# Kernel optimization log

Measured on AMD Instinct MI355X. Metric: run time of the kernel, lower is better.

Reference implementation:

```python
import jax, jax.numpy as jnp
import numpy as np

WIN = (7, 7)
NUM_HEADS = 12
LORA_SCALING = 16.0 / 16.0  # lora_alpha / lora_rank


def _relative_position_index(win):
    wh, ww = win
    coords = np.stack(np.meshgrid(np.arange(wh), np.arange(ww), indexing='ij'))  # (2, wh, ww)
    cf = coords.reshape(2, -1)
    rel = cf[:, :, None] - cf[:, None, :]  # (2, N, N)
    rel = rel.transpose(1, 2, 0)
    rel[:, :, 0] += wh - 1
    rel[:, :, 1] += ww - 1
    rel[:, :, 0] *= 2 * ww - 1
    return jnp.asarray(rel.sum(-1), dtype=jnp.int32)  # (N, N)


def setup_inputs() -> dict:
    key = jax.random.key(0)
    ks = jax.random.split(key, 12)
    B_, N, C, r = 2048, 49, 384, 16
    nW = 64
    s = 0.02
    return {
        'x': jax.random.normal(ks[0], (B_, N, C), jnp.float32),
        'mask': jnp.zeros((nW, N, N), jnp.float32),
        'qkv_w': jax.random.normal(ks[1], (C, 3 * C), jnp.float32) * s,
        'qkv_b': jax.random.normal(ks[2], (3 * C,), jnp.float32) * s,
        'qa_w': jax.random.normal(ks[3], (C, r), jnp.float32) * s,
        'qb_w': jax.random.normal(ks[4], (r, C), jnp.float32) * s,
        'va_w': jax.random.normal(ks[5], (C, r), jnp.float32) * s,
        'vb_w': jax.random.normal(ks[6], (r, C), jnp.float32) * s,
        'rpb_table': jax.random.normal(ks[7], ((2 * WIN[0] - 1) * (2 * WIN[1] - 1), NUM_HEADS), jnp.float32) * s,
        'proj_w': jax.random.normal(ks[8], (C, C), jnp.float32) * s,
        'proj_b': jax.random.normal(ks[9], (C,), jnp.float32) * s,
    }


def reference(x, mask, qkv_w, qkv_b, qa_w, qb_w, va_w, vb_w, rpb_table, proj_w, proj_b):
    B_, N, C = x.shape
    H = NUM_HEADS
    hd = C // H
    scale = hd ** -0.5

    qkv = (x @ qkv_w + qkv_b).reshape(B_, N, 3, H, hd)
    qkv = jnp.transpose(qkv, (2, 0, 3, 1, 4))  # (3, B_, H, N, hd)
    q, k, v = qkv[0], qkv[1], qkv[2]

    q_lora = LORA_SCALING * ((x @ qa_w) @ qb_w)  # (B_, N, C)
    q = q + jnp.transpose(q_lora.reshape(B_, N, H, hd), (0, 2, 1, 3))
    v_lora = LORA_SCALING * ((x @ va_w) @ vb_w)
    v = v + jnp.transpose(v_lora.reshape(B_, N, H, hd), (0, 2, 1, 3))

    attn = jnp.einsum('bhnd,bhmd->bhnm', q * scale, k)  # (B_, H, N, N)

    rel_idx = _relative_position_index(WIN)  # (N, N) static int
    rpb = rpb_table[rel_idx]  # (N, N, H)
    attn = attn + jnp.transpose(rpb, (2, 0, 1))[None]

    nW = mask.shape[0]
    attn = attn.reshape(B_ // nW, nW, H, N, N) + mask[None, :, None]
    attn = attn.reshape(B_, H, N, N)
    attn = jax.nn.softmax(attn, axis=-1)

    out = jnp.einsum('bhnm,bhmd->bhnd', attn, v)
    out = jnp.transpose(out, (0, 2, 1, 3)).reshape(B_, N, C)
    return out @ proj_w + proj_b
```

## Files before the change

kernel.cpp:

```cpp
#include <hip/hip_runtime.h>
#include <hip/hip_bf16.h>

typedef __hip_bfloat16 bf16;
typedef float f32x4 __attribute__((ext_vector_type(4)));
typedef short bf16x8 __attribute__((ext_vector_type(8)));

static __device__ __forceinline__ void gload_lds16(const void* g, void* l) {
    __builtin_amdgcn_global_load_lds(
        (const __attribute__((address_space(1))) void*)g,
        (__attribute__((address_space(3))) void*)l, 16, 0, 0);
}

static __device__ __forceinline__ short bf16bits(float v) {
    bf16 tb = __float2bfloat16(v);
    return *reinterpret_cast<short*>(&tb);
}

__global__ __launch_bounds__(256) void cvt_x_kernel(const float4* __restrict__ x,
                                                    bf16* __restrict__ xb, int n4) {
    int i = blockIdx.x * 256 + threadIdx.x;
    const int stride = gridDim.x * 256;
    for (; i < n4; i += stride) {
        float4 v = x[i];
        alignas(8) bf16 tmp[4];
        tmp[0] = __float2bfloat16(v.x);
        tmp[1] = __float2bfloat16(v.y);
        tmp[2] = __float2bfloat16(v.z);
        tmp[3] = __float2bfloat16(v.w);
        *reinterpret_cast<uint2*>(xb + 4l * i) = *reinterpret_cast<uint2*>(tmp);
    }
}

__global__ __launch_bounds__(256) void build_wefft_kernel(
    const float* __restrict__ qkv_w, const float* __restrict__ qa,
    const float* __restrict__ qb, const float* __restrict__ va,
    const float* __restrict__ vb, bf16* __restrict__ wt) {
    int idx = blockIdx.x * 256 + threadIdx.x;
    int ncol = idx / 384;
    int k = idx - ncol * 384;
    float v = qkv_w[k * 1152 + ncol];
    if (ncol < 384) {
        float s = 0.f;
#pragma unroll
        for (int j = 0; j < 16; ++j) s += qa[k * 16 + j] * qb[j * 384 + ncol];
        v += s;
    } else if (ncol >= 768) {
        int nc = ncol - 768;
        float s = 0.f;
#pragma unroll
        for (int j = 0; j < 16; ++j) s += va[k * 16 + j] * vb[j * 384 + nc];
        v += s;
    }
    wt[(long)ncol * 384 + k] = __float2bfloat16(v);
}

__global__ __launch_bounds__(256) void build_projt_kernel(const float* __restrict__ pw,
                                                          bf16* __restrict__ pt) {
    int idx = blockIdx.x * 256 + threadIdx.x;
    int ncol = idx / 384;
    int k = idx - ncol * 384;
    pt[(long)ncol * 384 + k] = __float2bfloat16(pw[k * 384 + ncol]);
}

__global__ __launch_bounds__(256) void build_cbias_kernel(const float* __restrict__ rpb_table,
                                                          const float* __restrict__ mask,
                                                          float* __restrict__ cbias) {
    int idx = blockIdx.x * 256 + threadIdx.x;
    int hw = idx / 2401;
    int ij = idx - hw * 2401;
    int h = hw >> 6, w = hw & 63;
    int i = ij / 49, j = ij - i * 49;
    int yi = i / 7, xi = i - yi * 7;
    int yj = j / 7, xj = j - yj * 7;
    int rel = (yi - yj + 6) * 13 + (xi - xj + 6);
    cbias[idx] = rpb_table[rel * 12 + h] + mask[w * 2401 + ij];
}

template <bool OUT_BF16>
__global__ __launch_bounds__(256) void gemm_kernel(const bf16* __restrict__ A,
                                                   const bf16* __restrict__ BT,
                                                   const float* __restrict__ bias,
                                                   void* __restrict__ Cout, int N, int K) {
    __shared__ short Al[128 * 32];
    __shared__ short Bl[128 * 32];
    const int t = threadIdx.x;
    const int lane = t & 63;
    const int wave = t >> 6;
    const int wr = wave >> 1;
    const int wc = wave & 1;
    const long rowBase = (long)blockIdx.y * 128;
    const long colBase = (long)blockIdx.x * 128;

    f32x4 acc[4][4];
#pragma unroll
    for (int m = 0; m < 4; ++m)
#pragma unroll
        for (int n = 0; n < 4; ++n) acc[m][n] = (f32x4){0.f, 0.f, 0.f, 0.f};

    const int r0 = t >> 2;
    const int kc0 = (t & 3) * 8;

    for (int k0 = 0; k0 < K; k0 += 32) {
        __syncthreads();
        gload_lds16(A + (rowBase + r0) * K + k0 + kc0, &Al[t * 8]);
        gload_lds16(A + (rowBase + r0 + 64) * K + k0 + kc0, &Al[(t + 256) * 8]);
        gload_lds16(BT + (colBase + r0) * K + k0 + kc0, &Bl[t * 8]);
        gload_lds16(BT + (colBase + r0 + 64) * K + k0 + kc0, &Bl[(t + 256) * 8]);
        asm volatile("s_waitcnt vmcnt(0)" ::: "memory");
        __syncthreads();

        bf16x8 af[4], bfr[4];
        const int rsel = (lane >> 4) * 8;
#pragma unroll
        for (int m = 0; m < 4; ++m)
            af[m] = *(const bf16x8*)&Al[(wr * 64 + m * 16 + (lane & 15)) * 32 + rsel];
#pragma unroll
        for (int n = 0; n < 4; ++n)
            bfr[n] = *(const bf16x8*)&Bl[(wc * 64 + n * 16 + (lane & 15)) * 32 + rsel];
#pragma unroll
        for (int m = 0; m < 4; ++m)
#pragma unroll
            for (int n = 0; n < 4; ++n)
                acc[m][n] = __builtin_amdgcn_mfma_f32_16x16x32_bf16(af[m], bfr[n],
                                                                    acc[m][n], 0, 0, 0);
    }

    const int crow0 = wr * 64 + ((t & 63) >> 4) * 4;
    const long ccol0 = colBase + wc * 64 + (lane & 15);
#pragma unroll
    for (int m = 0; m < 4; ++m) {
#pragma unroll
        for (int n = 0; n < 4; ++n) {
            const long col = ccol0 + n * 16;
            const float bv = bias[col];
#pragma unroll
            for (int r = 0; r < 4; ++r) {
                const long row = rowBase + crow0 + m * 16 + r;
                float v = acc[m][n][r] + bv;
                if (OUT_BF16)
                    ((bf16*)Cout)[row * N + col] = __float2bfloat16(v);
                else
                    ((float*)Cout)[row * N + col] = v;
            }
        }
    }
}

__global__ __launch_bounds__(256) void attn_kernel(const bf16* __restrict__ qkv,
                                                   const float* __restrict__ cbias,
                                                   bf16* __restrict__ out) {
    __shared__ short lds[4 * 7168];
    const int t = threadIdx.x, lane = t & 63, wave = t >> 6;
    short* W = lds + wave * 7168;
    const int bh = blockIdx.x * 4 + wave;
    const int b = bh / 12, h = bh - b * 12;
    const int g = lane >> 4, c = lane & 15;
    const int w = b & 63;

#pragma unroll
    for (int z = 0; z < 4; ++z)
        *(uint4*)&W[5120 + (z * 64 + lane) * 8] = (uint4){0u, 0u, 0u, 0u};

    const size_t base = (size_t)b * 49 * 1152 + h * 32;
    for (int c4 = lane; c4 < 196; c4 += 64) {
        int n = c4 >> 2, o = (c4 & 3) * 8;
        size_t gaddr = base + (size_t)n * 1152 + o;
        uint4 qv = *(const uint4*)&qkv[gaddr];
        uint4 kv = *(const uint4*)&qkv[gaddr + 384];
        uint4 vv = *(const uint4*)&qkv[gaddr + 768];
        *(uint4*)&W[n * 40 + o] = qv;
        *(uint4*)&W[2560 + n * 40 + o] = kv;
        alignas(16) short tmp[8];
        *(uint4*)tmp = vv;
#pragma unroll
        for (int j = 0; j < 8; ++j) {
            int d = o + j;
            W[5120 + ((d * 64 + n) ^ ((d & 7) << 3))] = tmp[j];
        }
    }
    __syncthreads();

    bf16x8 aq[4], bk[4];
#pragma unroll
    for (int mt = 0; mt < 4; ++mt) aq[mt] = *(const bf16x8*)&W[(mt * 16 + c) * 40 + g * 8];
#pragma unroll
    for (int nt = 0; nt < 4; ++nt) bk[nt] = *(const bf16x8*)&W[2560 + (nt * 16 + c) * 40 + g * 8];
    f32x4 S[4][4];
#pragma unroll
    for (int mt = 0; mt < 4; ++mt)
#pragma unroll
        for (int nt = 0; nt < 4; ++nt)
            S[mt][nt] = __builtin_amdgcn_mfma_f32_16x16x32_bf16(aq[mt], bk[nt],
                                                                (f32x4){0.f, 0.f, 0.f, 0.f}, 0, 0, 0);

    const float scale = 0.17677669529663687f;
    const float* cb = cbias + (size_t)((h << 6) | w) * 2401;
    float inv[16];
#pragma unroll
    for (int mt = 0; mt < 4; ++mt) {
#pragma unroll
        for (int nt = 0; nt < 4; ++nt) {
            int j = nt * 16 + c;
#pragma unroll
            for (int r = 0; r < 4; ++r) {
                int i = mt * 16 + g * 4 + r;
                float v = S[mt][nt][r] * scale;
                if (j < 49 && i < 49) v += cb[i * 49 + j];
                S[mt][nt][r] = (j < 49) ? v : -INFINITY;
            }
        }
#pragma unroll
        for (int r = 0; r < 4; ++r) {
            float m = fmaxf(fmaxf(S[mt][0][r], S[mt][1][r]), fmaxf(S[mt][2][r], S[mt][3][r]));
            m = fmaxf(m, __shfl_xor(m, 1));
            m = fmaxf(m, __shfl_xor(m, 2));
            m = fmaxf(m, __shfl_xor(m, 4));
            m = fmaxf(m, __shfl_xor(m, 8));
            float s = 0.f;
#pragma unroll
            for (int nt = 0; nt < 4; ++nt) {
                float e = __expf(S[mt][nt][r] - m);
                S[mt][nt][r] = e;
                s += e;
            }
            s += __shfl_xor(s, 1);
            s += __shfl_xor(s, 2);
            s += __shfl_xor(s, 4);
            s += __shfl_xor(s, 8);
            inv[mt * 4 + r] = 1.f / s;
        }
    }

    __syncthreads();
#pragma unroll
    for (int mt = 0; mt < 4; ++mt)
#pragma unroll
        for (int nt = 0; nt < 4; ++nt)
#pragma unroll
            for (int r = 0; r < 4; ++r) {
                int i = mt * 16 + g * 4 + r, j = nt * 16 + c;
                W[(i * 64 + j) ^ ((i & 7) << 3)] = bf16bits(S[mt][nt][r]);
            }
    __syncthreads();

    f32x4 O[4][2];
#pragma unroll
    for (int mt = 0; mt < 4; ++mt)
#pragma unroll
        for (int dt = 0; dt < 2; ++dt) O[mt][dt] = (f32x4){0.f, 0.f, 0.f, 0.f};
#pragma unroll
    for (int ks = 0; ks < 2; ++ks) {
        bf16x8 pa[4], vb2[2];
#pragma unroll
        for (int mt = 0; mt < 4; ++mt) {
            int i = mt * 16 + c;
            pa[mt] = *(const bf16x8*)&W[(i * 64 + ks * 32 + g * 8) ^ ((i & 7) << 3)];
        }
#pragma unroll
        for (int dt = 0; dt < 2; ++dt) {
            int d = dt * 16 + c;
            vb2[dt] = *(const bf16x8*)&W[5120 + ((d * 64 + ks * 32 + g * 8) ^ ((d & 7) << 3))];
        }
#pragma unroll
        for (int mt = 0; mt < 4; ++mt)
#pragma unroll
            for (int dt = 0; dt < 2; ++dt)
                O[mt][dt] = __builtin_amdgcn_mfma_f32_16x16x32_bf16(pa[mt], vb2[dt],
                                                                    O[mt][dt], 0, 0, 0);
    }

#pragma unroll
    for (int mt = 0; mt < 4; ++mt)
#pragma unroll
        for (int r = 0; r < 4; ++r) {
            int i = mt * 16 + g * 4 + r;
            if (i < 49) {
#pragma unroll
                for (int dt = 0; dt < 2; ++dt) {
                    int d = dt * 16 + c;
                    out[((size_t)(b * 49 + i)) * 384 + h * 32 + d] =
                        __float2bfloat16(O[mt][dt][r] * inv[mt * 4 + r]);
                }
            }
        }
}

extern "C" void kernel_launch(void* const* d_in, const int* in_sizes, int n_in,
                              void* d_out, int out_size, void* d_ws, size_t ws_size,
                              hipStream_t stream) {
    (void)in_sizes; (void)n_in; (void)out_size; (void)ws_size;
    const float* x      = (const float*)d_in[0];
    const float* mask   = (const float*)d_in[1];
    const float* qkv_w  = (const float*)d_in[2];
    const float* qkv_b  = (const float*)d_in[3];
    const float* qa_w   = (const float*)d_in[4];
    const float* qb_w   = (const float*)d_in[5];
    const float* va_w   = (const float*)d_in[6];
    const float* vb_w   = (const float*)d_in[7];
    const float* rpb    = (const float*)d_in[8];
    const float* proj_w = (const float*)d_in[9];
    const float* proj_b = (const float*)d_in[10];

    char* ws = (char*)d_ws;
    bf16* xb    = (bf16*)(ws);
    bf16* wefft = (bf16*)(ws + 77070336);
    bf16* projt = (bf16*)(ws + 77955072);
    bf16* qkv   = (bf16*)(ws + 78249984);
    bf16* attno = (bf16*)(ws + 309460992);
    float* cbias = (float*)(ws);

    cvt_x_kernel<<<2048, 256, 0, stream>>>((const float4*)x, xb, 9633792);
    build_wefft_kernel<<<1728, 256, 0, stream>>>(qkv_w, qa_w, qb_w, va_w, vb_w, wefft);
    build_projt_kernel<<<576, 256, 0, stream>>>(proj_w, projt);
    gemm_kernel<true><<<dim3(9, 784), 256, 0, stream>>>(xb, wefft, qkv_b, qkv, 1152, 384);
    build_cbias_kernel<<<7203, 256, 0, stream>>>(rpb, mask, cbias);
    attn_kernel<<<6144, 256, 0, stream>>>(qkv, cbias, attno);
    gemm_kernel<false><<<dim3(3, 784), 256, 0, stream>>>(attno, projt, proj_b, d_out, 384, 384);
}
```

Measured before the change: 432.4 us.

## Fuse fp32-to-bf16 x conversion into QKV GEMM with swizzled K=64 tiles

Removes the standalone x conversion kernel: the QKV GEMM now reads fp32 x directly and converts it to bf16 while staging into LDS. The GEMM K-tile grows from 32 to 64, and LDS uses an XOR swizzle to avoid bank conflicts. Workgroup IDs are remapped across 8 groups, likely so that placement suits the XCDs. This saves a full write and re-read of the bf16 copy of x, at the cost of register-path loads for A instead of direct-to-LDS loads. The workspace layout is reorganised to match.

```diff
diff --git a/kernel.cpp b/kernel.cpp
--- a/kernel.cpp
+++ b/kernel.cpp
@@ -14,21 +14,6 @@
 static __device__ __forceinline__ short bf16bits(float v) {
     bf16 tb = __float2bfloat16(v);
     return *reinterpret_cast<short*>(&tb);
-}
-
-__global__ __launch_bounds__(256) void cvt_x_kernel(const float4* __restrict__ x,
-                                                    bf16* __restrict__ xb, int n4) {
-    int i = blockIdx.x * 256 + threadIdx.x;
-    const int stride = gridDim.x * 256;
-    for (; i < n4; i += stride) {
-        float4 v = x[i];
-        alignas(8) bf16 tmp[4];
-        tmp[0] = __float2bfloat16(v.x);
-        tmp[1] = __float2bfloat16(v.y);
-        tmp[2] = __float2bfloat16(v.z);
-        tmp[3] = __float2bfloat16(v.w);
-        *reinterpret_cast<uint2*>(xb + 4l * i) = *reinterpret_cast<uint2*>(tmp);
-    }
 }
 
 __global__ __launch_bounds__(256) void build_wefft_kernel(
@@ -76,20 +61,27 @@
     cbias[idx] = rpb_table[rel * 12 + h] + mask[w * 2401 + ij];
 }
 
-template <bool OUT_BF16>
-__global__ __launch_bounds__(256) void gemm_kernel(const bf16* __restrict__ A,
+template <bool A_FP32, bool OUT_BF16>
+__global__ __launch_bounds__(256) void gemm_kernel(const void* __restrict__ Av,
                                                    const bf16* __restrict__ BT,
                                                    const float* __restrict__ bias,
-                                                   void* __restrict__ Cout, int N, int K) {
-    __shared__ short Al[128 * 32];
-    __shared__ short Bl[128 * 32];
+                                                   void* __restrict__ Cout,
+                                                   int N, int K, int nxb, int nwg) {
+    __shared__ short Al[128 * 64];
+    __shared__ short Bl[128 * 64];
     const int t = threadIdx.x;
     const int lane = t & 63;
     const int wave = t >> 6;
     const int wr = wave >> 1;
     const int wc = wave & 1;
-    const long rowBase = (long)blockIdx.y * 128;
-    const long colBase = (long)blockIdx.x * 128;
+    const int g = lane >> 4, c = lane & 15;
+
+    const int q8 = nwg >> 3;
+    const int wgid = (blockIdx.x & 7) * q8 + (blockIdx.x >> 3);
+    const int by = wgid / nxb;
+    const int bx = wgid - by * nxb;
+    const long rowBase = (long)by * 128;
+    const long colBase = (long)bx * 128;
 
     f32x4 acc[4][4];
 #pragma unroll
@@ -97,36 +89,71 @@
 #pragma unroll
         for (int n = 0; n < 4; ++n) acc[m][n] = (f32x4){0.f, 0.f, 0.f, 0.f};
 
-    const int r0 = t >> 2;
-    const int kc0 = (t & 3) * 8;
-
-    for (int k0 = 0; k0 < K; k0 += 32) {
+    for (int k0 = 0; k0 < K; k0 += 64) {
         __syncthreads();
-        gload_lds16(A + (rowBase + r0) * K + k0 + kc0, &Al[t * 8]);
-        gload_lds16(A + (rowBase + r0 + 64) * K + k0 + kc0, &Al[(t + 256) * 8]);
-        gload_lds16(BT + (colBase + r0) * K + k0 + kc0, &Bl[t * 8]);
-        gload_lds16(BT + (colBase + r0 + 64) * K + k0 + kc0, &Bl[(t + 256) * 8]);
+#pragma unroll
+        for (int it = 0; it < 4; ++it) {
+            int chunk = it * 256 + t;
+            int row = chunk >> 3;
+            int blk = lane & 7;
+            gload_lds16(BT + (size_t)(colBase + row) * K + k0 + ((blk ^ (row & 7)) * 8),
+                        &Bl[(it * 256 + wave * 64) * 8]);
+        }
+        if (A_FP32) {
+            const float* Af = (const float*)Av;
+#pragma unroll
+            for (int it = 0; it < 4; ++it) {
+                int chunk = it * 256 + t;
+                int row = chunk >> 3;
+                int blk = chunk & 7;
+                const float* src = Af + (size_t)(rowBase + row) * K + k0 + ((blk ^ (row & 7)) * 8);
+                float4 v0 = *(const float4*)src;
+                float4 v1 = *(const float4*)(src + 4);
+                alignas(16) short tmp[8];
+                tmp[0] = bf16bits(v0.x); tmp[1] = bf16bits(v0.y);
+                tmp[2] = bf16bits(v0.z); tmp[3] = bf16bits(v0.w);
+                tmp[4] = bf16bits(v1.x); tmp[5] = bf16bits(v1.y);
+                tmp[6] = bf16bits(v1.z); tmp[7] = bf16bits(v1.w);
+                *(uint4*)&Al[chunk * 8] = *(const uint4*)tmp;
+            }
+        } else {
+            const bf16* Ab = (const bf16*)Av;
+#pragma unroll
+            for (int it = 0; it < 4; ++it) {
+                int chunk = it * 256 + t;
+                int row = chunk >> 3;
+                int blk = lane & 7;
+                gload_lds16(Ab + (size_t)(rowBase + row) * K + k0 + ((blk ^ (row & 7)) * 8),
+                            &Al[(it * 256 + wave * 64) * 8]);
+            }
+        }
         asm volatile("s_waitcnt vmcnt(0)" ::: "memory");
         __syncthreads();
 
-        bf16x8 af[4], bfr[4];
-        const int rsel = (lane >> 4) * 8;
-#pragma unroll
-        for (int m = 0; m < 4; ++m)
-            af[m] = *(const bf16x8*)&Al[(wr * 64 + m * 16 + (lane & 15)) * 32 + rsel];
-#pragma unroll
-        for (int n = 0; n < 4; ++n)
-            bfr[n] = *(const bf16x8*)&Bl[(wc * 64 + n * 16 + (lane & 15)) * 32 + rsel];
-#pragma unroll
-        for (int m = 0; m < 4; ++m)
-#pragma unroll
-            for (int n = 0; n < 4; ++n)
-                acc[m][n] = __builtin_amdgcn_mfma_f32_16x16x32_bf16(af[m], bfr[n],
-                                                                    acc[m][n], 0, 0, 0);
-    }
-
-    const int crow0 = wr * 64 + ((t & 63) >> 4) * 4;
-    const long ccol0 = colBase + wc * 64 + (lane & 15);
+#pragma unroll
+        for (int ks = 0; ks < 2; ++ks) {
+            bf16x8 af[4], bfr[4];
+#pragma unroll
+            for (int m = 0; m < 4; ++m) {
+                int row = wr * 64 + m * 16 + c;
+                af[m] = *(const bf16x8*)&Al[row * 64 + (((ks * 4 + g) ^ (c & 7)) * 8)];
+            }
+#pragma unroll
+            for (int n = 0; n < 4; ++n) {
+                int row = wc * 64 + n * 16 + c;
+                bfr[n] = *(const bf16x8*)&Bl[row * 64 + (((ks * 4 + g) ^ (c & 7)) * 8)];
+            }
+#pragma unroll
+            for (int m = 0; m < 4; ++m)
+#pragma unroll
+                for (int n = 0; n < 4; ++n)
+                    acc[m][n] = __builtin_amdgcn_mfma_f32_16x16x32_bf16(af[m], bfr[n],
+                                                                        acc[m][n], 0, 0, 0);
+        }
+    }
+
+    const int crow0 = wr * 64 + g * 4;
+    const long ccol0 = colBase + wc * 64 + c;
 #pragma unroll
     for (int m = 0; m < 4; ++m) {
 #pragma unroll
@@ -302,18 +329,16 @@
     const float* proj_b = (const float*)d_in[10];
 
     char* ws = (char*)d_ws;
-    bf16* xb    = (bf16*)(ws);
-    bf16* wefft = (bf16*)(ws + 77070336);
-    bf16* projt = (bf16*)(ws + 77955072);
-    bf16* qkv   = (bf16*)(ws + 78249984);
-    bf16* attno = (bf16*)(ws + 309460992);
-    float* cbias = (float*)(ws);
-
-    cvt_x_kernel<<<2048, 256, 0, stream>>>((const float4*)x, xb, 9633792);
+    bf16* wefft  = (bf16*)(ws);
+    bf16* projt  = (bf16*)(ws + 884736);
+    float* cbias = (float*)(ws + 1179648);
+    bf16* qkv    = (bf16*)(ws + 8555520);
+    bf16* attno  = (bf16*)(ws + 239766528);
+
     build_wefft_kernel<<<1728, 256, 0, stream>>>(qkv_w, qa_w, qb_w, va_w, vb_w, wefft);
     build_projt_kernel<<<576, 256, 0, stream>>>(proj_w, projt);
-    gemm_kernel<true><<<dim3(9, 784), 256, 0, stream>>>(xb, wefft, qkv_b, qkv, 1152, 384);
     build_cbias_kernel<<<7203, 256, 0, stream>>>(rpb, mask, cbias);
+    gemm_kernel<true, true><<<7056, 256, 0, stream>>>(x, wefft, qkv_b, qkv, 1152, 384, 9, 7056);
     attn_kernel<<<6144, 256, 0, stream>>>(qkv, cbias, attno);
-    gemm_kernel<false><<<dim3(3, 784), 256, 0, stream>>>(attno, projt, proj_b, d_out, 384, 384);
-}
+    gemm_kernel<false, false><<<2352, 256, 0, stream>>>(attno, projt, proj_b, d_out, 384, 384, 3, 2352);
+}
```

Result: faster. 407.7 us (-5.7%).
